# Kernel tuning notes

Hardware: AMD Instinct MI355X
Metric: run time of the kernel (lower is better)

The kernel has to match this reference:

```python
import itertools
import jax, jax.numpy as jnp
import numpy as np

N_BLOCKS = 2_097_152  # number of 8x8 blocks; 512 MB fp32 input


def _make_alpha():
    a = np.array([1.0 / np.sqrt(2)] + [1.0] * 7)
    return jnp.asarray(np.outer(a, a), dtype=jnp.float32)  # [8,8]


def _make_dct_tensor():
    t = np.zeros((8, 8, 8, 8), dtype=np.float32)
    for x, y, u, v in itertools.product(range(8), repeat=4):
        t[x, y, u, v] = np.cos((2 * u + 1) * x * np.pi / 16) * np.cos((2 * v + 1) * y * np.pi / 16)
    return jnp.asarray(t)  # [8,8,8,8]


def setup_inputs() -> dict:
    key = jax.random.key(0)
    image = jax.random.normal(key, (N_BLOCKS, 8, 8), dtype=jnp.float32)
    return {"image": image, "alpha": _make_alpha(), "dct_tensor": _make_dct_tensor()}


def reference(image, alpha, dct_tensor):
    # result[n,u,v] = 0.25 * sum_{x,y} (image[n,x,y] * alpha[x,y]) * T[x,y,u,v] + 128
    scaled = image * alpha  # broadcast over batch of 8x8 blocks
    out = 0.25 * jnp.einsum("nxy,xyuv->nuv", scaled, dct_tensor) + 128.0
    return out
```

## Files before the change

kernel.cpp:

```cpp
#include <hip/hip_runtime.h>


#define WG      256
#define BPW     (WG / 8)
#define SETS    2
#define BLKWG   (SETS * BPW)
#define STRIDE4 17

__global__ __launch_bounds__(WG, 8) void dct8x8_kernel(
    const float* __restrict__ image,
    const float* __restrict__ alpha,
    const float* __restrict__ dct,
    float* __restrict__ out,
    int nblocks)
{
    __shared__ float4 lds4[SETS * BPW * STRIDE4];

    const int t = threadIdx.x;
    const int b = t >> 3;
    const int r = t & 7;
    const int lane = t & 63;

    float mv;
    {
        const int i = lane >> 3, j = lane & 7;
        mv = 0.5f * alpha[i * 8 + 1] * dct[i * 512 + j * 8];
    }
    float M[64];
#pragma unroll
    for (int k = 0; k < 64; ++k)
        M[k] = __int_as_float(__builtin_amdgcn_readlane(__float_as_int(mv), k));

    float mu[8];
#pragma unroll
    for (int x = 0; x < 8; ++x)
        mu[x] = 0.5f * alpha[x * 8 + 1] * dct[x * 512 + r * 8];

    const float4* __restrict__ in4 = (const float4*)image;
    float4* __restrict__ o4 = (float4*)out;

    const long long wgbase = (long long)blockIdx.x * BLKWG;

    float4 lo[SETS], hi[SETS];
#pragma unroll
    for (int s = 0; s < SETS; ++s) {
        const long long gblk = wgbase + s * BPW + b;
        if (gblk < nblocks) {
            const size_t p = (size_t)gblk * 16 + r * 2;
            lo[s] = in4[p];
            hi[s] = in4[p + 1];
        } else {
            lo[s] = make_float4(0.f, 0.f, 0.f, 0.f);
            hi[s] = lo[s];
        }
    }

#pragma unroll
    for (int s = 0; s < SETS; ++s) {
        const float row[8] = {lo[s].x, lo[s].y, lo[s].z, lo[s].w,
                              hi[s].x, hi[s].y, hi[s].z, hi[s].w};
        float P[8];
#pragma unroll
        for (int v = 0; v < 8; ++v) {
            float acc = 0.0f;
#pragma unroll
            for (int y = 0; y < 8; ++y)
                acc = fmaf(row[y], M[y * 8 + v], acc);
            P[v] = acc;
        }
        float4* buf = &lds4[s * (BPW * STRIDE4)];
        buf[b * STRIDE4 + r * 2 + 0] = make_float4(P[0], P[1], P[2], P[3]);
        buf[b * STRIDE4 + r * 2 + 1] = make_float4(P[4], P[5], P[6], P[7]);
    }
    __syncthreads();

#pragma unroll
    for (int s = 0; s < SETS; ++s) {
        const float4* buf = &lds4[s * (BPW * STRIDE4)];
        float O[8] = {128.f, 128.f, 128.f, 128.f, 128.f, 128.f, 128.f, 128.f};
#pragma unroll
        for (int x = 0; x < 8; ++x) {
            const float4 plo = buf[b * STRIDE4 + x * 2 + 0];
            const float4 phi = buf[b * STRIDE4 + x * 2 + 1];
            const float m = mu[x];
            O[0] = fmaf(m, plo.x, O[0]);
            O[1] = fmaf(m, plo.y, O[1]);
            O[2] = fmaf(m, plo.z, O[2]);
            O[3] = fmaf(m, plo.w, O[3]);
            O[4] = fmaf(m, phi.x, O[4]);
            O[5] = fmaf(m, phi.y, O[5]);
            O[6] = fmaf(m, phi.z, O[6]);
            O[7] = fmaf(m, phi.w, O[7]);
        }
        const long long gblk = wgbase + s * BPW + b;
        if (gblk < nblocks) {
            const size_t p = (size_t)gblk * 16 + r * 2;
            o4[p]     = make_float4(O[0], O[1], O[2], O[3]);
            o4[p + 1] = make_float4(O[4], O[5], O[6], O[7]);
        }
    }
}

extern "C" void kernel_launch(void* const* d_in, const int* in_sizes, int n_in,
                              void* d_out, int out_size, void* d_ws, size_t ws_size,
                              hipStream_t stream) {
    const float* image = (const float*)d_in[0];
    const float* alpha = (const float*)d_in[1];
    const float* dct   = (const float*)d_in[2];
    float* outp = (float*)d_out;

    const int nblocks = in_sizes[0] / 64;
    const long long wgs = ((long long)nblocks + BLKWG - 1) / BLKWG;

    dct8x8_kernel<<<(int)wgs, WG, 0, stream>>>(image, alpha, dct, outp, nblocks);
}
```

Measured before the change: 214.0 us.

## Make DCT kernel persistent with register prefetch of next tile

Result: slower. 705.0 us (+229.4%).

```diff
diff --git a/kernel.cpp b/kernel.cpp
--- a/kernel.cpp
+++ b/kernel.cpp
@@ -2,10 +2,11 @@
 
 
 #define WG      256
-#define BPW     (WG / 8)
+#define BPW     32
 #define SETS    2
 #define BLKWG   (SETS * BPW)
 #define STRIDE4 17
+#define MAXWG   2048
 
 __global__ __launch_bounds__(WG, 8) void dct8x8_kernel(
     const float* __restrict__ image,
@@ -39,65 +40,82 @@
     const float4* __restrict__ in4 = (const float4*)image;
     float4* __restrict__ o4 = (float4*)out;
 
-    const long long wgbase = (long long)blockIdx.x * BLKWG;
+    const long long ntiles = ((long long)nblocks + BLKWG - 1) / BLKWG;
+    long long tile = blockIdx.x;
+    if (tile >= ntiles) return;
 
-    float4 lo[SETS], hi[SETS];
-#pragma unroll
-    for (int s = 0; s < SETS; ++s) {
-        const long long gblk = wgbase + s * BPW + b;
-        if (gblk < nblocks) {
-            const size_t p = (size_t)gblk * 16 + r * 2;
-            lo[s] = in4[p];
-            hi[s] = in4[p + 1];
-        } else {
-            lo[s] = make_float4(0.f, 0.f, 0.f, 0.f);
-            hi[s] = lo[s];
-        }
+    float4 c0lo = make_float4(0.f,0.f,0.f,0.f), c0hi = c0lo, c1lo = c0lo, c1hi = c0lo;
+    {
+        const long long g0 = tile * BLKWG + b;
+        const long long g1 = g0 + BPW;
+        if (g0 < nblocks) { const size_t p = (size_t)g0 * 16 + r * 2; c0lo = in4[p]; c0hi = in4[p+1]; }
+        if (g1 < nblocks) { const size_t p = (size_t)g1 * 16 + r * 2; c1lo = in4[p]; c1hi = in4[p+1]; }
     }
 
-#pragma unroll
-    for (int s = 0; s < SETS; ++s) {
-        const float row[8] = {lo[s].x, lo[s].y, lo[s].z, lo[s].w,
-                              hi[s].x, hi[s].y, hi[s].z, hi[s].w};
-        float P[8];
-#pragma unroll
-        for (int v = 0; v < 8; ++v) {
-            float acc = 0.0f;
-#pragma unroll
-            for (int y = 0; y < 8; ++y)
-                acc = fmaf(row[y], M[y * 8 + v], acc);
-            P[v] = acc;
+    while (true) {
+        const long long nxt = tile + gridDim.x;
+        const bool have_nxt = nxt < ntiles;
+        float4 n0lo = make_float4(0.f,0.f,0.f,0.f), n0hi = n0lo, n1lo = n0lo, n1hi = n0lo;
+        if (have_nxt) {
+            const long long g0 = nxt * BLKWG + b;
+            const long long g1 = g0 + BPW;
+            if (g0 < nblocks) { const size_t p = (size_t)g0 * 16 + r * 2; n0lo = in4[p]; n0hi = in4[p+1]; }
+            if (g1 < nblocks) { const size_t p = (size_t)g1 * 16 + r * 2; n1lo = in4[p]; n1hi = in4[p+1]; }
         }
-        float4* buf = &lds4[s * (BPW * STRIDE4)];
-        buf[b * STRIDE4 + r * 2 + 0] = make_float4(P[0], P[1], P[2], P[3]);
-        buf[b * STRIDE4 + r * 2 + 1] = make_float4(P[4], P[5], P[6], P[7]);
-    }
-    __syncthreads();
 
 #pragma unroll
-    for (int s = 0; s < SETS; ++s) {
-        const float4* buf = &lds4[s * (BPW * STRIDE4)];
-        float O[8] = {128.f, 128.f, 128.f, 128.f, 128.f, 128.f, 128.f, 128.f};
+        for (int s = 0; s < SETS; ++s) {
+            const float4 vlo = s ? c1lo : c0lo;
+            const float4 vhi = s ? c1hi : c0hi;
+            const float row[8] = {vlo.x, vlo.y, vlo.z, vlo.w,
+                                  vhi.x, vhi.y, vhi.z, vhi.w};
+            float P[8];
 #pragma unroll
-        for (int x = 0; x < 8; ++x) {
-            const float4 plo = buf[b * STRIDE4 + x * 2 + 0];
-            const float4 phi = buf[b * STRIDE4 + x * 2 + 1];
-            const float m = mu[x];
-            O[0] = fmaf(m, plo.x, O[0]);
-            O[1] = fmaf(m, plo.y, O[1]);
-            O[2] = fmaf(m, plo.z, O[2]);
-            O[3] = fmaf(m, plo.w, O[3]);
-            O[4] = fmaf(m, phi.x, O[4]);
-            O[5] = fmaf(m, phi.y, O[5]);
-            O[6] = fmaf(m, phi.z, O[6]);
-            O[7] = fmaf(m, phi.w, O[7]);
+            for (int v = 0; v < 8; ++v) {
+                float acc = 0.0f;
+#pragma unroll
+                for (int y = 0; y < 8; ++y)
+                    acc = fmaf(row[y], M[y * 8 + v], acc);
+                P[v] = acc;
+            }
+            float4* buf = &lds4[s * (BPW * STRIDE4)];
+            buf[b * STRIDE4 + r * 2 + 0] = make_float4(P[0], P[1], P[2], P[3]);
+            buf[b * STRIDE4 + r * 2 + 1] = make_float4(P[4], P[5], P[6], P[7]);
         }
-        const long long gblk = wgbase + s * BPW + b;
-        if (gblk < nblocks) {
-            const size_t p = (size_t)gblk * 16 + r * 2;
-            o4[p]     = make_float4(O[0], O[1], O[2], O[3]);
-            o4[p + 1] = make_float4(O[4], O[5], O[6], O[7]);
+
+        asm volatile("s_waitcnt lgkmcnt(0)" ::: "memory");
+
+#pragma unroll
+        for (int s = 0; s < SETS; ++s) {
+            const float4* buf = &lds4[s * (BPW * STRIDE4)];
+            float O[8] = {128.f,128.f,128.f,128.f,128.f,128.f,128.f,128.f};
+#pragma unroll
+            for (int x = 0; x < 8; ++x) {
+                const float4 plo = buf[b * STRIDE4 + x * 2 + 0];
+                const float4 phi = buf[b * STRIDE4 + x * 2 + 1];
+                const float m = mu[x];
+                O[0] = fmaf(m, plo.x, O[0]);
+                O[1] = fmaf(m, plo.y, O[1]);
+                O[2] = fmaf(m, plo.z, O[2]);
+                O[3] = fmaf(m, plo.w, O[3]);
+                O[4] = fmaf(m, phi.x, O[4]);
+                O[5] = fmaf(m, phi.y, O[5]);
+                O[6] = fmaf(m, phi.z, O[6]);
+                O[7] = fmaf(m, phi.w, O[7]);
+            }
+            const long long gblk = tile * BLKWG + s * BPW + b;
+            if (gblk < nblocks) {
+                const size_t p = (size_t)gblk * 16 + r * 2;
+                o4[p]     = make_float4(O[0], O[1], O[2], O[3]);
+                o4[p + 1] = make_float4(O[4], O[5], O[6], O[7]);
+            }
         }
+
+        asm volatile("" ::: "memory");
+
+        if (!have_nxt) break;
+        c0lo = n0lo; c0hi = n0hi; c1lo = n1lo; c1hi = n1hi;
+        tile = nxt;
     }
 }
 
@@ -110,7 +128,9 @@
     float* outp = (float*)d_out;
 
     const int nblocks = in_sizes[0] / 64;
-    const long long wgs = ((long long)nblocks + BLKWG - 1) / BLKWG;
+    const long long ntiles = ((long long)nblocks + BLKWG - 1) / BLKWG;
+    int grid = (int)((ntiles < MAXWG) ? ntiles : MAXWG);
+    if (grid < 1) grid = 1;
 
-    dct8x8_kernel<<<(int)wgs, WG, 0, stream>>>(image, alpha, dct, outp, nblocks);
+    dct8x8_kernel<<<grid, WG, 0, stream>>>(image, alpha, dct, outp, nblocks);
 }
```

## Make LDS transpose wave-local, drop workgroup barrier, process more blocks per thread

Applied to the files above, without the earlier changes.

Measured after the change: 203.9 us. 1.05x faster.

```diff
diff --git a/kernel.cpp b/kernel.cpp
--- a/kernel.cpp
+++ b/kernel.cpp
@@ -2,24 +2,33 @@
 
 
 #define WG      256
-#define BPW     (WG / 8)
-#define SETS    2
-#define BLKWG   (SETS * BPW)
+#define SETS    4
+#define BLKWAVE 32
+#define BLKWG   128
 #define STRIDE4 17
 
-__global__ __launch_bounds__(WG, 8) void dct8x8_kernel(
-    const float* __restrict__ image,
-    const float* __restrict__ alpha,
-    const float* __restrict__ dct,
-    float* __restrict__ out,
-    int nblocks)
+template<bool FULL>
+__device__ __forceinline__ void process_tile(
+    const float4* __restrict__ in4, float4* __restrict__ o4,
+    float4* __restrict__ lds4, const float* __restrict__ alpha,
+    const float* __restrict__ dct, long long wgbase, int nblocks,
+    int w, int b8, int r, int lane)
 {
-    __shared__ float4 lds4[SETS * BPW * STRIDE4];
+    const long long myblk0 = wgbase + w * BLKWAVE + b8;
 
-    const int t = threadIdx.x;
-    const int b = t >> 3;
-    const int r = t & 7;
-    const int lane = t & 63;
+    float4 lo[SETS], hi[SETS];
+#pragma unroll
+    for (int s = 0; s < SETS; ++s) {
+        const long long g = myblk0 + s * 8;
+        if (FULL || g < nblocks) {
+            const size_t p = (size_t)g * 16 + r * 2;
+            lo[s] = in4[p];
+            hi[s] = in4[p + 1];
+        } else {
+            lo[s] = make_float4(0.f, 0.f, 0.f, 0.f);
+            hi[s] = lo[s];
+        }
+    }
 
     float mv;
     {
@@ -36,25 +45,6 @@
     for (int x = 0; x < 8; ++x)
         mu[x] = 0.5f * alpha[x * 8 + 1] * dct[x * 512 + r * 8];
 
-    const float4* __restrict__ in4 = (const float4*)image;
-    float4* __restrict__ o4 = (float4*)out;
-
-    const long long wgbase = (long long)blockIdx.x * BLKWG;
-
-    float4 lo[SETS], hi[SETS];
-#pragma unroll
-    for (int s = 0; s < SETS; ++s) {
-        const long long gblk = wgbase + s * BPW + b;
-        if (gblk < nblocks) {
-            const size_t p = (size_t)gblk * 16 + r * 2;
-            lo[s] = in4[p];
-            hi[s] = in4[p + 1];
-        } else {
-            lo[s] = make_float4(0.f, 0.f, 0.f, 0.f);
-            hi[s] = lo[s];
-        }
-    }
-
 #pragma unroll
     for (int s = 0; s < SETS; ++s) {
         const float row[8] = {lo[s].x, lo[s].y, lo[s].z, lo[s].w,
@@ -68,20 +58,21 @@
                 acc = fmaf(row[y], M[y * 8 + v], acc);
             P[v] = acc;
         }
-        float4* buf = &lds4[s * (BPW * STRIDE4)];
-        buf[b * STRIDE4 + r * 2 + 0] = make_float4(P[0], P[1], P[2], P[3]);
-        buf[b * STRIDE4 + r * 2 + 1] = make_float4(P[4], P[5], P[6], P[7]);
+        float4* buf = &lds4[(w * BLKWAVE + s * 8 + b8) * STRIDE4];
+        buf[r * 2 + 0] = make_float4(P[0], P[1], P[2], P[3]);
+        buf[r * 2 + 1] = make_float4(P[4], P[5], P[6], P[7]);
     }
-    __syncthreads();
+
+    asm volatile("s_waitcnt lgkmcnt(0)" ::: "memory");
 
 #pragma unroll
     for (int s = 0; s < SETS; ++s) {
-        const float4* buf = &lds4[s * (BPW * STRIDE4)];
+        const float4* buf = &lds4[(w * BLKWAVE + s * 8 + b8) * STRIDE4];
         float O[8] = {128.f, 128.f, 128.f, 128.f, 128.f, 128.f, 128.f, 128.f};
 #pragma unroll
         for (int x = 0; x < 8; ++x) {
-            const float4 plo = buf[b * STRIDE4 + x * 2 + 0];
-            const float4 phi = buf[b * STRIDE4 + x * 2 + 1];
+            const float4 plo = buf[x * 2 + 0];
+            const float4 phi = buf[x * 2 + 1];
             const float m = mu[x];
             O[0] = fmaf(m, plo.x, O[0]);
             O[1] = fmaf(m, plo.y, O[1]);
@@ -92,12 +83,38 @@
             O[6] = fmaf(m, phi.z, O[6]);
             O[7] = fmaf(m, phi.w, O[7]);
         }
-        const long long gblk = wgbase + s * BPW + b;
-        if (gblk < nblocks) {
-            const size_t p = (size_t)gblk * 16 + r * 2;
+        const long long g = myblk0 + s * 8;
+        if (FULL || g < nblocks) {
+            const size_t p = (size_t)g * 16 + r * 2;
             o4[p]     = make_float4(O[0], O[1], O[2], O[3]);
             o4[p + 1] = make_float4(O[4], O[5], O[6], O[7]);
         }
+    }
+}
+
+__global__ __launch_bounds__(WG, 4) void dct8x8_kernel(
+    const float* __restrict__ image,
+    const float* __restrict__ alpha,
+    const float* __restrict__ dct,
+    float* __restrict__ out,
+    int nblocks)
+{
+    __shared__ float4 lds4[BLKWG * STRIDE4];
+
+    const int t = threadIdx.x;
+    const int w = t >> 6;
+    const int lane = t & 63;
+    const int b8 = lane >> 3;
+    const int r = lane & 7;
+
+    const long long wgbase = (long long)blockIdx.x * BLKWG;
+    const float4* in4 = (const float4*)image;
+    float4* o4 = (float4*)out;
+
+    if (wgbase + BLKWG <= (long long)nblocks) {
+        process_tile<true >(in4, o4, lds4, alpha, dct, wgbase, nblocks, w, b8, r, lane);
+    } else {
+        process_tile<false>(in4, o4, lds4, alpha, dct, wgbase, nblocks, w, b8, r, lane);
     }
 }
 
```
